# Performance work log

Measured on AMD Instinct MI355X. Metric: run time of the kernel, lower is better.

## Reference

```python
import jax, jax.numpy as jnp
import numpy as np

H = 1024
B = 8
S = 2048

def setup_inputs() -> dict:
    key = jax.random.key(0)
    ks = jax.random.split(key, 16)
    w = lambda k, shp: (jax.random.normal(k, shp, dtype=jnp.float32) * 0.02)
    return {
        "hidden_states": jax.random.normal(ks[0], (B, S, H), dtype=jnp.float32),
        "context_vector": jax.random.normal(ks[1], (B, H), dtype=jnp.float32),
        # nn.Linear weights stored torch-style as [out, in]
        "Wq": w(ks[2], (H, H)), "bq": w(ks[3], (H,)),
        "Wk": w(ks[4], (H, H)), "bk": w(ks[5], (H,)),
        "Wv": w(ks[6], (H, H)), "bv": w(ks[7], (H,)),
        "Wcq": w(ks[8], (H, H)),  # only .weight.t() used in original (no bias)
        "Wck": w(ks[9], (H, H)),
        "g_qh": jax.random.normal(ks[10], (H, 1), dtype=jnp.float32),
        "g_kh": jax.random.normal(ks[11], (H, 1), dtype=jnp.float32),
        "g_qc": jax.random.normal(ks[12], (H, 1), dtype=jnp.float32),
        "g_kc": jax.random.normal(ks[13], (H, 1), dtype=jnp.float32),
    }

def reference(hidden_states, context_vector, Wq, bq, Wk, bk, Wv, bv, Wcq, Wck, g_qh, g_kh, g_qc, g_kc):
    # Linear projections (torch Linear: x @ W.T + b)
    query = jnp.einsum('bsh,oh->bso', hidden_states, Wq) + bq   # [B,S,H]
    key_  = jnp.einsum('bsh,oh->bso', hidden_states, Wk) + bk
    value = jnp.einsum('bsh,oh->bso', hidden_states, Wv) + bv

    # gate = sigmoid(Q @ g_h + (ctx @ g_c)[:,None,:])  -> [B,S,1]
    q_gate = jax.nn.sigmoid(query @ g_qh + (context_vector @ g_qc)[:, None, :])
    k_gate = jax.nn.sigmoid(key_  @ g_kh + (context_vector @ g_kc)[:, None, :])

    # context projections: ctx @ weight.t() (no bias in original usage) -> [B,1,H]
    ctx_q = (context_vector @ Wcq.T)[:, None, :]
    ctx_k = (context_vector @ Wck.T)[:, None, :]

    query_hat = (1.0 - q_gate) * query + q_gate * ctx_q
    key_hat   = (1.0 - k_gate) * key_  + k_gate * ctx_k

    scale = 1.0 / jnp.sqrt(jnp.asarray(H, dtype=jnp.float32))
    scores = jnp.einsum('bqh,bkh->bqk', query_hat, key_hat) * scale  # [B,S,S]
    probs = jax.nn.softmax(scores, axis=-1)
    output = jnp.einsum('bqk,bkh->bqh', probs, value)  # [B,S,H]
    return (output, scores)
```

## Files before the change

kernel.cpp:

```cpp
#include <hip/hip_runtime.h>
#include <cstdint>
#include <cstddef>

#define H 1024
#define NB 8
#define S 2048
#define MROWS (NB*S)

using short8 = __attribute__((ext_vector_type(8))) short;
using f32x4  = __attribute__((ext_vector_type(4))) float;

__device__ __forceinline__ unsigned short f2bf(float f){
  union { float f; unsigned int u; } c; c.f = f;
  unsigned int u = c.u;
  return (unsigned short)((u + 0x7fffu + ((u >> 16) & 1u)) >> 16);
}


__global__ void k_cvt3(const float* __restrict__ a, const float* __restrict__ b, const float* __restrict__ c,
                       unsigned short* __restrict__ oa, unsigned short* __restrict__ ob, unsigned short* __restrict__ oc){
  const float* src = blockIdx.y == 0 ? a : (blockIdx.y == 1 ? b : c);
  unsigned short* dst = blockIdx.y == 0 ? oa : (blockIdx.y == 1 ? ob : oc);
  int i = (blockIdx.x * 256 + threadIdx.x) * 4;
  float4 v = *reinterpret_cast<const float4*>(src + i);
  ushort4 o;
  o.x = f2bf(v.x); o.y = f2bf(v.y); o.z = f2bf(v.z); o.w = f2bf(v.w);
  *reinterpret_cast<ushort4*>(dst + i) = o;
}

__global__ void k_colproj(const float* __restrict__ Wq_, const float* __restrict__ gq_,
                          const float* __restrict__ Wk_, const float* __restrict__ gk_,
                          float* __restrict__ up){
  const float* W = blockIdx.z ? Wk_ : Wq_;
  const float* g = blockIdx.z ? gk_ : gq_;
  const int in = blockIdx.x * 256 + threadIdx.x;
  const int o0 = blockIdx.y * 128;
  float s = 0.f;
  for (int o = 0; o < 128; ++o) s = fmaf(W[(size_t)(o0 + o) * H + in], g[o0 + o], s);
  up[(blockIdx.z * 8 + blockIdx.y) * 1024 + in] = s;
}

__global__ void k_ucombine(const float* __restrict__ up, float* __restrict__ uq, float* __restrict__ uk){
  int i = blockIdx.x * 256 + threadIdx.x;
  int m = i >> 10, j = i & 1023;
  float s = 0.f;
  #pragma unroll
  for (int c = 0; c < 8; ++c) s += up[(m * 8 + c) * 1024 + j];
  (m ? uk : uq)[j] = s;
}

__global__ __launch_bounds__(256) void k_ctxproj(const float* __restrict__ Wcq, const float* __restrict__ Wck,
    const float* __restrict__ ctx, float* __restrict__ outq, float* __restrict__ outk){
  __shared__ float cs[NB * H];
  const float* W = blockIdx.y ? Wck : Wcq;
  float* out = blockIdx.y ? outk : outq;
  const int t = threadIdx.x;
  for (int i = t; i < NB * H; i += 256) cs[i] = ctx[i];
  __syncthreads();
  const int wid = t >> 6, lane = t & 63;
  const int row = blockIdx.x * 4 + wid;
  float a[NB];
  #pragma unroll
  for (int b = 0; b < NB; ++b) a[b] = 0.f;
  for (int i0 = 0; i0 < H; i0 += 64){
    const float w = W[(size_t)row * H + i0 + lane];
    #pragma unroll
    for (int b = 0; b < NB; ++b) a[b] = fmaf(w, cs[b * H + i0 + lane], a[b]);
  }
  #pragma unroll
  for (int b = 0; b < NB; ++b){
    float v = a[b];
    #pragma unroll
    for (int off = 32; off > 0; off >>= 1) v += __shfl_xor(v, off);
    if (lane == 0) out[b * H + row] = v;
  }
}

__device__ float block_dot(const float* a, const float* b, float* red, int t){
  float s = 0.f;
  for (int i = t; i < H; i += 256) s = fmaf(a[i], b[i], s);
  red[t] = s;
  __syncthreads();
  for (int off = 128; off > 0; off >>= 1){
    if (t < off) red[t] += red[t + off];
    __syncthreads();
  }
  float r = red[0];
  __syncthreads();
  return r;
}

__global__ void k_scalars(const float* __restrict__ bq, const float* __restrict__ gqh,
                          const float* __restrict__ bk, const float* __restrict__ gkh,
                          const float* __restrict__ ctx, const float* __restrict__ gqc,
                          const float* __restrict__ gkc, float* __restrict__ scal){
  __shared__ float red[256];
  const int t = threadIdx.x;
  float v;
  v = block_dot(bq, gqh, red, t); if (t == 0) scal[0] = v;
  v = block_dot(bk, gkh, red, t); if (t == 0) scal[1] = v;
  for (int b = 0; b < NB; ++b){
    v = block_dot(ctx + b * H, gqc, red, t); if (t == 0) scal[2 + b] = v;
    v = block_dot(ctx + b * H, gkc, red, t); if (t == 0) scal[10 + b] = v;
  }
}

__global__ __launch_bounds__(256) void k_prepass(const float* __restrict__ hs,
    const float* __restrict__ u_q, const float* __restrict__ u_k, const float* __restrict__ scal,
    unsigned short* __restrict__ hsb, float* __restrict__ gq, float* __restrict__ gk){
  const int t = threadIdx.x, wid = t >> 6, lane = t & 63;
  const int row = blockIdx.x * 4 + wid;
  const float* hrow = hs + (size_t)row * H;
  unsigned short* orow = hsb + (size_t)row * H;
  float sq = 0.f, sk = 0.f;
  #pragma unroll
  for (int c = 0; c < 4; ++c){
    const int idx = (lane + c * 64) * 4;
    float4 v  = *reinterpret_cast<const float4*>(hrow + idx);
    float4 uq = *reinterpret_cast<const float4*>(u_q + idx);
    float4 uk = *reinterpret_cast<const float4*>(u_k + idx);
    ushort4 o; o.x = f2bf(v.x); o.y = f2bf(v.y); o.z = f2bf(v.z); o.w = f2bf(v.w);
    *reinterpret_cast<ushort4*>(orow + idx) = o;
    sq += v.x*uq.x + v.y*uq.y + v.z*uq.z + v.w*uq.w;
    sk += v.x*uk.x + v.y*uk.y + v.z*uk.z + v.w*uk.w;
  }
  #pragma unroll
  for (int off = 32; off > 0; off >>= 1){
    sq += __shfl_xor(sq, off);
    sk += __shfl_xor(sk, off);
  }
  if (lane == 0){
    const int b = row >> 11;
    gq[row] = 1.f / (1.f + __expf(-(sq + scal[0] + scal[2 + b])));
    gk[row] = 1.f / (1.f + __expf(-(sk + scal[1] + scal[10 + b])));
  }
}


#define STG(bufi, opi, halfi, koff, P0, P1) \
  { __builtin_amdgcn_global_load_lds((const __attribute__((address_space(1))) void*)(P0 + (koff)), \
      (__attribute__((address_space(3))) void*)((char*)(&lds[bufi][opi][halfi][0]) + (wid*2+0)*1024), 16, 0, 0); \
    __builtin_amdgcn_global_load_lds((const __attribute__((address_space(1))) void*)(P1 + (koff)), \
      (__attribute__((address_space(3))) void*)((char*)(&lds[bufi][opi][halfi][0]) + (wid*2+1)*1024), 16, 0, 0); }
#define STG_A(bufi, halfi, koff) STG(bufi, 0, halfi, koff, sA0, sA1)
#define STG_B(bufi, halfi, koff) STG(bufi, 1, halfi, koff, sB0, sB1)

#define DS_A(bufi, ks, mh) \
  { _Pragma("unroll") for (int m_ = 0; m_ < 4; ++m_){ \
      const int ar_ = wr*128 + ((mh)*4 + m_)*16 + (lane & 15); \
      const int sl_ = (lane >> 4) ^ ((ar_ >> 1) & 3); \
      af[m_] = *reinterpret_cast<const short8*>(&lds[bufi][0][ks][ar_*32 + sl_*8]); } }
#define DS_B(bufi, ks) \
  { _Pragma("unroll") for (int n_ = 0; n_ < 4; ++n_){ \
      const int br_ = wc*64 + n_*16 + (lane & 15); \
      const int sl_ = (lane >> 4) ^ ((br_ >> 1) & 3); \
      bf[n_] = *reinterpret_cast<const short8*>(&lds[bufi][1][ks][br_*32 + sl_*8]); } }
#define MFMA16(mh) \
  { __builtin_amdgcn_s_setprio(1); \
    _Pragma("unroll") for (int m_ = 0; m_ < 4; ++m_) \
      _Pragma("unroll") for (int n_ = 0; n_ < 4; ++n_) \
        acc[(mh)*4 + m_][n_] = __builtin_amdgcn_mfma_f32_16x16x32_bf16(af[m_], bf[n_], acc[(mh)*4 + m_][n_], 0, 0, 0); \
    __builtin_amdgcn_s_setprio(0); }
#define VM4() asm volatile("s_waitcnt vmcnt(4)" ::: "memory");
#define VM0() asm volatile("s_waitcnt vmcnt(0)" ::: "memory");
#define BAR() { asm volatile("" ::: "memory"); __builtin_amdgcn_s_barrier(); asm volatile("" ::: "memory"); }

template<int MODE>
__global__ __launch_bounds__(512, 2)
void k_gemm(const unsigned short* __restrict__ A, const unsigned short* __restrict__ B,
            int K, int ldA, int ldB, long long Abatch, long long Bbatch,
            const float* __restrict__ gate, const float* __restrict__ bias,
            const float* __restrict__ ctxv,
            unsigned short* __restrict__ outb, float* __restrict__ outf,
            long long outBatch, float scale)
{
  __shared__ __align__(16) short lds[2][2][2][8192];

  const int t = threadIdx.x;
  const int wid = t >> 6, lane = t & 63;
  const int wr = wid >> 2, wc = wid & 3;
  const int bz = blockIdx.z;
  const unsigned short* Ab = A + (size_t)bz * (size_t)Abatch;
  const unsigned short* Bb = B + (size_t)bz * (size_t)Bbatch;
  const int row0 = blockIdx.x * 256;
  const int col0 = blockIdx.y * 256;

  const int c0 = (wid*2 + 0)*64 + lane;
  const int c1 = (wid*2 + 1)*64 + lane;
  const int r0s = c0 >> 2, r1s = c1 >> 2;
  const int kc0 = (c0 & 3) ^ ((r0s >> 1) & 3);
  const int kc1 = (c1 & 3) ^ ((r1s >> 1) & 3);
  const unsigned short* sA0 = Ab + (size_t)(row0 + r0s) * (size_t)ldA + kc0*8;
  const unsigned short* sA1 = Ab + (size_t)(row0 + r1s) * (size_t)ldA + kc1*8;
  const unsigned short* sB0 = Bb + (size_t)(col0 + r0s) * (size_t)ldB + kc0*8;
  const unsigned short* sB1 = Bb + (size_t)(col0 + r1s) * (size_t)ldB + kc1*8;

  f32x4 acc[8][4] = {};
  short8 af[4], bf[4];

  STG_A(0, 0, 0); STG_B(0, 0, 0); STG_A(0, 1, 32); STG_B(0, 1, 32);
  VM0(); BAR();

  const int niter = K >> 7;
  for (int it = 0; it < niter; ++it){
    const int t1k = (it*2 + 1) << 6;
    const int t2k = (it*2 + 2) << 6;
    const bool more = (it + 1 < niter);
    DS_A(0, 0, 0); DS_B(0, 0); STG_A(1, 0, t1k); MFMA16(0); BAR();
    DS_A(0, 0, 1); STG_B(1, 0, t1k); MFMA16(1); VM4(); BAR();
    DS_A(0, 1, 0); DS_B(0, 1); STG_A(1, 1, t1k + 32); MFMA16(0); BAR();
    DS_A(0, 1, 1); STG_B(1, 1, t1k + 32); MFMA16(1);
    if (more) { VM4(); } else { VM0(); }
    BAR();
    DS_A(1, 0, 0); DS_B(1, 0); if (more) STG_A(0, 0, t2k); MFMA16(0); BAR();
    DS_A(1, 0, 1); if (more) { STG_B(0, 0, t2k); } MFMA16(1); if (more) VM4(); BAR();
    DS_A(1, 1, 0); DS_B(1, 1); if (more) STG_A(0, 1, t2k + 32); MFMA16(0); BAR();
    DS_A(1, 1, 1); if (more) { STG_B(0, 1, t2k + 32); } MFMA16(1); if (more) VM4(); BAR();
  }

  if constexpr (MODE == 0 || MODE == 1){
    const int b = row0 >> 11;
    #pragma unroll
    for (int mi = 0; mi < 8; ++mi)
      #pragma unroll
      for (int n = 0; n < 4; ++n)
        #pragma unroll
        for (int r = 0; r < 4; ++r){
          const int grow = row0 + wr*128 + mi*16 + (lane >> 4)*4 + r;
          const int gcol = col0 + wc*64 + n*16 + (lane & 15);
          const float g = gate[grow];
          const float q = acc[mi][n][r] + bias[gcol];
          outb[(size_t)grow * H + gcol] = f2bf((1.f - g) * q + g * ctxv[b * H + gcol]);
        }
  } else if constexpr (MODE == 2){
    short* tp = (short*)lds;
    const int bb = row0 >> 11;
    const int s0 = row0 & (S - 1);
    #pragma unroll
    for (int ci = 0; ci < 2; ++ci)
      #pragma unroll
      for (int cj = 0; cj < 2; ++cj){
        __syncthreads();
        if (wr == ci && (wc >> 1) == cj){
          const int lc0 = (wc & 1) * 64;
          #pragma unroll
          for (int mi = 0; mi < 8; ++mi)
            #pragma unroll
            for (int n = 0; n < 4; ++n)
              #pragma unroll
              for (int r = 0; r < 4; ++r){
                const int lr = mi*16 + (lane >> 4)*4 + r;
                const int lc = lc0 + n*16 + (lane & 15);
                tp[lr*129 + lc] = (short)f2bf(acc[mi][n][r] + bias[col0 + cj*128 + lc]);
              }
        }
        __syncthreads();
        const int hl = t >> 2;
        const int sb = (t & 3) * 32;
        unsigned short* vout = outb + (size_t)bb * H * S + (size_t)(col0 + cj*128 + hl) * S
                                    + (size_t)(s0 + ci*128 + sb);
        #pragma unroll
        for (int i2 = 0; i2 < 32; i2 += 4){
          ushort4 o;
          o.x = (unsigned short)tp[(sb + i2 + 0)*129 + hl];
          o.y = (unsigned short)tp[(sb + i2 + 1)*129 + hl];
          o.z = (unsigned short)tp[(sb + i2 + 2)*129 + hl];
          o.w = (unsigned short)tp[(sb + i2 + 3)*129 + hl];
          *reinterpret_cast<ushort4*>(vout + i2) = o;
        }
      }
  } else if constexpr (MODE == 3){
    #pragma unroll
    for (int mi = 0; mi < 8; ++mi)
      #pragma unroll
      for (int n = 0; n < 4; ++n)
        #pragma unroll
        for (int r = 0; r < 4; ++r){
          const int grow = row0 + wr*128 + mi*16 + (lane >> 4)*4 + r;
          const int gcol = col0 + wc*64 + n*16 + (lane & 15);
          outf[(size_t)bz * (size_t)outBatch + (size_t)grow * S + gcol] = acc[mi][n][r] * scale;
        }
  } else {
    #pragma unroll
    for (int mi = 0; mi < 8; ++mi)
      #pragma unroll
      for (int n = 0; n < 4; ++n)
        #pragma unroll
        for (int r = 0; r < 4; ++r){
          const int grow = row0 + wr*128 + mi*16 + (lane >> 4)*4 + r;
          const int gcol = col0 + wc*64 + n*16 + (lane & 15);
          outf[(size_t)bz * (size_t)outBatch + (size_t)grow * H + gcol] = acc[mi][n][r];
        }
  }
}

__global__ __launch_bounds__(256) void k_softmax(const float* __restrict__ scores,
                                                 unsigned short* __restrict__ probs){
  const int row = blockIdx.x;
  const float* srow = scores + (size_t)row * S;
  unsigned short* prow = probs + (size_t)row * S;
  const int t = threadIdx.x, wid = t >> 6, lane = t & 63;
  __shared__ float red[8];
  float4 v0 = *reinterpret_cast<const float4*>(srow + t * 4);
  float4 v1 = *reinterpret_cast<const float4*>(srow + 1024 + t * 4);
  float m = fmaxf(fmaxf(fmaxf(v0.x, v0.y), fmaxf(v0.z, v0.w)),
                  fmaxf(fmaxf(v1.x, v1.y), fmaxf(v1.z, v1.w)));
  #pragma unroll
  for (int off = 32; off > 0; off >>= 1) m = fmaxf(m, __shfl_xor(m, off));
  if (lane == 0) red[wid] = m;
  __syncthreads();
  m = fmaxf(fmaxf(red[0], red[1]), fmaxf(red[2], red[3]));
  float4 e0, e1;
  e0.x = __expf(v0.x - m); e0.y = __expf(v0.y - m); e0.z = __expf(v0.z - m); e0.w = __expf(v0.w - m);
  e1.x = __expf(v1.x - m); e1.y = __expf(v1.y - m); e1.z = __expf(v1.z - m); e1.w = __expf(v1.w - m);
  float s = (e0.x + e0.y + e0.z + e0.w) + (e1.x + e1.y + e1.z + e1.w);
  #pragma unroll
  for (int off = 32; off > 0; off >>= 1) s += __shfl_xor(s, off);
  if (lane == 0) red[4 + wid] = s;
  __syncthreads();
  s = (red[4] + red[5]) + (red[6] + red[7]);
  const float inv = 1.f / s;
  ushort4 o;
  o.x = f2bf(e0.x * inv); o.y = f2bf(e0.y * inv); o.z = f2bf(e0.z * inv); o.w = f2bf(e0.w * inv);
  *reinterpret_cast<ushort4*>(prow + t * 4) = o;
  o.x = f2bf(e1.x * inv); o.y = f2bf(e1.y * inv); o.z = f2bf(e1.z * inv); o.w = f2bf(e1.w * inv);
  *reinterpret_cast<ushort4*>(prow + 1024 + t * 4) = o;
}

extern "C" void kernel_launch(void* const* d_in, const int* in_sizes, int n_in,
                              void* d_out, int out_size, void* d_ws, size_t ws_size,
                              hipStream_t stream) {
  const float* hs  = (const float*)d_in[0];
  const float* ctx = (const float*)d_in[1];
  const float* Wq  = (const float*)d_in[2];
  const float* bq  = (const float*)d_in[3];
  const float* Wk  = (const float*)d_in[4];
  const float* bk  = (const float*)d_in[5];
  const float* Wv  = (const float*)d_in[6];
  const float* bv  = (const float*)d_in[7];
  const float* Wcq = (const float*)d_in[8];
  const float* Wck = (const float*)d_in[9];
  const float* gqh = (const float*)d_in[10];
  const float* gkh = (const float*)d_in[11];
  const float* gqc = (const float*)d_in[12];
  const float* gkc = (const float*)d_in[13];

  char* ws = (char*)d_ws;
  const size_t T = (size_t)MROWS * H * 2;
  unsigned short* hsb  = (unsigned short*)(ws);
  unsigned short* qhat = (unsigned short*)(ws + T);
  unsigned short* khat = (unsigned short*)(ws + 2 * T);
  unsigned short* vt   = (unsigned short*)(ws + 3 * T);
  unsigned short* wqb  = (unsigned short*)(ws + 4 * T);
  unsigned short* wkb  = (unsigned short*)(ws + 4 * T + 2097152);
  unsigned short* wvb  = (unsigned short*)(ws + 4 * T + 4194304);
  float* fb    = (float*)(ws + 4 * T + 6291456);
  float* u_q   = fb;
  float* u_k   = fb + 1024;
  float* ctxq  = fb + 2048;
  float* ctxk  = fb + 10240;
  float* gq    = fb + 18432;
  float* gk    = fb + 34816;
  float* scal  = fb + 51200;
  float* u_part= fb + 51232;
  unsigned short* probs = (unsigned short*)ws;

  float* out_attn   = (float*)d_out;
  float* out_scores = out_attn + (size_t)MROWS * H;

  k_cvt3<<<dim3(1024, 3), 256, 0, stream>>>(Wq, Wk, Wv, wqb, wkb, wvb);
  k_colproj<<<dim3(4, 8, 2), 256, 0, stream>>>(Wq, gqh, Wk, gkh, u_part);
  k_ucombine<<<8, 256, 0, stream>>>(u_part, u_q, u_k);
  k_ctxproj<<<dim3(256, 2), 256, 0, stream>>>(Wcq, Wck, ctx, ctxq, ctxk);
  k_scalars<<<1, 256, 0, stream>>>(bq, gqh, bk, gkh, ctx, gqc, gkc, scal);
  k_prepass<<<MROWS / 4, 256, 0, stream>>>(hs, u_q, u_k, scal, hsb, gq, gk);

  k_gemm<0><<<dim3(64, 4, 1), 512, 0, stream>>>(hsb, wqb, 1024, 1024, 1024, 0, 0,
      gq, bq, ctxq, qhat, nullptr, 0, 1.f);
  k_gemm<1><<<dim3(64, 4, 1), 512, 0, stream>>>(hsb, wkb, 1024, 1024, 1024, 0, 0,
      gk, bk, ctxk, khat, nullptr, 0, 1.f);
  k_gemm<2><<<dim3(64, 4, 1), 512, 0, stream>>>(hsb, wvb, 1024, 1024, 1024, 0, 0,
      nullptr, bv, nullptr, vt, nullptr, 0, 1.f);

  k_gemm<3><<<dim3(8, 8, 8), 512, 0, stream>>>(qhat, khat, 1024, 1024, 1024,
      (long long)S * H, (long long)S * H, nullptr, nullptr, nullptr,
      nullptr, out_scores, (long long)S * S, 0.03125f);

  k_softmax<<<MROWS, 256, 0, stream>>>(out_scores, probs);

  k_gemm<4><<<dim3(8, 4, 8), 512, 0, stream>>>(probs, vt, 2048, 2048, 2048,
      (long long)S * S, (long long)H * S, nullptr, nullptr, nullptr,
      nullptr, out_attn, (long long)S * H, 1.f);
}
```

Baseline: 357.0 us.

## Refactor gated QK scores algebraically via Wq^T Wk product to drop a projection GEMM

Rewrites scores = q_hat·k_hat^T by expanding the gated blends into a main term hs·(Wq^T Wk)·hs^T plus rank-one corrections built from per-row and per-column scalars. A small GEMM computes M = Wq^T Wk once, then one big GEMM forms T = hs·M, replacing the separate Q and K projection GEMMs. The scores GEMM uses hs directly as the second operand and applies the corrections in its epilogue. It adds several small precompute kernels and changes the bf16 rounding path, since hs is rounded before M is applied, which may shift numerical error.

```diff
diff --git a/kernel.cpp b/kernel.cpp
--- a/kernel.cpp
+++ b/kernel.cpp
@@ -17,10 +17,7 @@
 }
 
 
-__global__ void k_cvt3(const float* __restrict__ a, const float* __restrict__ b, const float* __restrict__ c,
-                       unsigned short* __restrict__ oa, unsigned short* __restrict__ ob, unsigned short* __restrict__ oc){
-  const float* src = blockIdx.y == 0 ? a : (blockIdx.y == 1 ? b : c);
-  unsigned short* dst = blockIdx.y == 0 ? oa : (blockIdx.y == 1 ? ob : oc);
+__global__ void k_cvt1(const float* __restrict__ src, unsigned short* __restrict__ dst){
   int i = (blockIdx.x * 256 + threadIdx.x) * 4;
   float4 v = *reinterpret_cast<const float4*>(src + i);
   ushort4 o;
@@ -28,25 +25,55 @@
   *reinterpret_cast<ushort4*>(dst + i) = o;
 }
 
-__global__ void k_colproj(const float* __restrict__ Wq_, const float* __restrict__ gq_,
-                          const float* __restrict__ Wk_, const float* __restrict__ gk_,
-                          float* __restrict__ up){
-  const float* W = blockIdx.z ? Wk_ : Wq_;
-  const float* g = blockIdx.z ? gk_ : gq_;
+__global__ __launch_bounds__(256) void k_transpose(const float* __restrict__ Wq_, const float* __restrict__ Wk_,
+    unsigned short* __restrict__ Wqt_, unsigned short* __restrict__ Wkt_){
+  const float* src = blockIdx.z ? Wk_ : Wq_;
+  unsigned short* dst = blockIdx.z ? Wkt_ : Wqt_;
+  __shared__ unsigned short tl[64][65];
+  const int t = threadIdx.x;
+  const int bx = blockIdx.x, by = blockIdx.y;
+  const int co = (t & 15) * 4;
+  #pragma unroll
+  for (int pass = 0; pass < 4; ++pass){
+    const int ro = (t >> 4) + pass * 16;
+    float4 v = *reinterpret_cast<const float4*>(src + (size_t)(by*64 + ro) * H + bx*64 + co);
+    tl[co + 0][ro] = f2bf(v.x);
+    tl[co + 1][ro] = f2bf(v.y);
+    tl[co + 2][ro] = f2bf(v.z);
+    tl[co + 3][ro] = f2bf(v.w);
+  }
+  __syncthreads();
+  #pragma unroll
+  for (int pass = 0; pass < 4; ++pass){
+    const int hh = (t >> 4) + pass * 16;
+    const int oo = (t & 15) * 4;
+    ushort4 w;
+    w.x = tl[hh][oo + 0]; w.y = tl[hh][oo + 1]; w.z = tl[hh][oo + 2]; w.w = tl[hh][oo + 3];
+    *reinterpret_cast<ushort4*>(dst + (size_t)(bx*64 + hh) * H + by*64 + oo) = w;
+  }
+}
+
+__global__ void k_colproj(const float* __restrict__ Wq_, const float* __restrict__ Wk_,
+                          const float* __restrict__ gqh, const float* __restrict__ gkh,
+                          const float* __restrict__ bq, const float* __restrict__ bk,
+                          float* __restrict__ up4){
+  const int z = blockIdx.z;
+  const float* W = (z == 0 || z == 2) ? Wq_ : Wk_;
+  const float* g = (z == 0) ? gqh : (z == 1) ? gkh : (z == 2) ? bk : bq;
   const int in = blockIdx.x * 256 + threadIdx.x;
   const int o0 = blockIdx.y * 128;
   float s = 0.f;
   for (int o = 0; o < 128; ++o) s = fmaf(W[(size_t)(o0 + o) * H + in], g[o0 + o], s);
-  up[(blockIdx.z * 8 + blockIdx.y) * 1024 + in] = s;
-}
-
-__global__ void k_ucombine(const float* __restrict__ up, float* __restrict__ uq, float* __restrict__ uk){
+  up4[(z * 8 + blockIdx.y) * 1024 + in] = s;
+}
+
+__global__ void k_ucombine4(const float* __restrict__ up4, float* __restrict__ u4){
   int i = blockIdx.x * 256 + threadIdx.x;
-  int m = i >> 10, j = i & 1023;
+  int z = i >> 10, h = i & 1023;
   float s = 0.f;
   #pragma unroll
-  for (int c = 0; c < 8; ++c) s += up[(m * 8 + c) * 1024 + j];
-  (m ? uk : uq)[j] = s;
+  for (int c = 0; c < 8; ++c) s += up4[(z * 8 + c) * 1024 + h];
+  u4[i] = s;
 }
 
 __global__ __launch_bounds__(256) void k_ctxproj(const float* __restrict__ Wcq, const float* __restrict__ Wck,
@@ -76,63 +103,114 @@
   }
 }
 
-__device__ float block_dot(const float* a, const float* b, float* red, int t){
+__global__ __launch_bounds__(256) void k_colproj8(const float* __restrict__ Wq_, const float* __restrict__ Wk_,
+    const float* __restrict__ ctxq, const float* __restrict__ ctxk, float* __restrict__ up8){
+  __shared__ float cs[NB * 128];
+  const int z = blockIdx.z;
+  const float* W = z ? Wk_ : Wq_;
+  const float* g = z ? ctxq : ctxk;
+  const int t = threadIdx.x;
+  const int o0 = blockIdx.y * 128;
+  for (int i = t; i < NB * 128; i += 256){
+    int b = i >> 7, oo = i & 127;
+    cs[i] = g[b * H + o0 + oo];
+  }
+  __syncthreads();
+  const int h = blockIdx.x * 256 + t;
+  float s[NB];
+  #pragma unroll
+  for (int b = 0; b < NB; ++b) s[b] = 0.f;
+  for (int oo = 0; oo < 128; ++oo){
+    const float w = W[(size_t)(o0 + oo) * H + h];
+    #pragma unroll
+    for (int b = 0; b < NB; ++b) s[b] = fmaf(w, cs[b * 128 + oo], s[b]);
+  }
+  #pragma unroll
+  for (int b = 0; b < NB; ++b)
+    up8[z * 65536 + blockIdx.y * 8192 + b * 1024 + h] = s[b];
+}
+
+__global__ void k_ucombine8(const float* __restrict__ up8, float* __restrict__ uXY){
+  int i = blockIdx.x * 256 + threadIdx.x;
+  int z = i >> 13, rem = i & 8191;
   float s = 0.f;
-  for (int i = t; i < H; i += 256) s = fmaf(a[i], b[i], s);
-  red[t] = s;
-  __syncthreads();
-  for (int off = 128; off > 0; off >>= 1){
-    if (t < off) red[t] += red[t + off];
-    __syncthreads();
-  }
-  float r = red[0];
-  __syncthreads();
-  return r;
-}
-
-__global__ void k_scalars(const float* __restrict__ bq, const float* __restrict__ gqh,
-                          const float* __restrict__ bk, const float* __restrict__ gkh,
-                          const float* __restrict__ ctx, const float* __restrict__ gqc,
-                          const float* __restrict__ gkc, float* __restrict__ scal){
-  __shared__ float red[256];
-  const int t = threadIdx.x;
-  float v;
-  v = block_dot(bq, gqh, red, t); if (t == 0) scal[0] = v;
-  v = block_dot(bk, gkh, red, t); if (t == 0) scal[1] = v;
-  for (int b = 0; b < NB; ++b){
-    v = block_dot(ctx + b * H, gqc, red, t); if (t == 0) scal[2 + b] = v;
-    v = block_dot(ctx + b * H, gkc, red, t); if (t == 0) scal[10 + b] = v;
+  #pragma unroll
+  for (int y = 0; y < 8; ++y) s += up8[z * 65536 + y * 8192 + rem];
+  uXY[i] = s;
+}
+
+__global__ __launch_bounds__(512) void k_scalars(const float* __restrict__ bq, const float* __restrict__ gqh,
+    const float* __restrict__ bk, const float* __restrict__ gkh,
+    const float* __restrict__ ctx, const float* __restrict__ gqc, const float* __restrict__ gkc,
+    const float* __restrict__ ctxq, const float* __restrict__ ctxk, float* __restrict__ scal){
+  const int wid = threadIdx.x >> 6, lane = threadIdx.x & 63;
+  for (int d = wid; d < 43; d += 8){
+    const float *pa, *pb;
+    if (d == 0){ pa = bq; pb = gqh; }
+    else if (d == 1){ pa = bk; pb = gkh; }
+    else if (d < 10){ pa = ctx + (d - 2) * H; pb = gqc; }
+    else if (d < 18){ pa = ctx + (d - 10) * H; pb = gkc; }
+    else if (d == 18){ pa = bq; pb = bk; }
+    else if (d < 27){ pa = bq; pb = ctxk + (d - 19) * H; }
+    else if (d < 35){ pa = ctxq + (d - 27) * H; pb = bk; }
+    else { pa = ctxq + (d - 35) * H; pb = ctxk + (d - 35) * H; }
+    float s = 0.f;
+    for (int i = lane; i < H; i += 64) s = fmaf(pa[i], pb[i], s);
+    #pragma unroll
+    for (int off = 32; off > 0; off >>= 1) s += __shfl_xor(s, off);
+    if (lane == 0) scal[d] = s;
   }
 }
 
 __global__ __launch_bounds__(256) void k_prepass(const float* __restrict__ hs,
-    const float* __restrict__ u_q, const float* __restrict__ u_k, const float* __restrict__ scal,
-    unsigned short* __restrict__ hsb, float* __restrict__ gq, float* __restrict__ gk){
+    const float* __restrict__ u4, const float* __restrict__ uXY, const float* __restrict__ scal,
+    unsigned short* __restrict__ hsb, float* __restrict__ Prow, float* __restrict__ Qcol){
   const int t = threadIdx.x, wid = t >> 6, lane = t & 63;
   const int row = blockIdx.x * 4 + wid;
+  const int b = row >> 11;
   const float* hrow = hs + (size_t)row * H;
+  const float* u_q = u4;
+  const float* u_k = u4 + 1024;
+  const float* aq  = u4 + 2048;
+  const float* ak  = u4 + 3072;
+  const float* uXb = uXY + b * 1024;
+  const float* uYb = uXY + 8192 + b * 1024;
   unsigned short* orow = hsb + (size_t)row * H;
-  float sq = 0.f, sk = 0.f;
+  float d1 = 0.f, d2 = 0.f, d3 = 0.f, d4 = 0.f, d5 = 0.f, d6 = 0.f;
   #pragma unroll
   for (int c = 0; c < 4; ++c){
     const int idx = (lane + c * 64) * 4;
     float4 v  = *reinterpret_cast<const float4*>(hrow + idx);
-    float4 uq = *reinterpret_cast<const float4*>(u_q + idx);
-    float4 uk = *reinterpret_cast<const float4*>(u_k + idx);
+    float4 a1 = *reinterpret_cast<const float4*>(u_q + idx);
+    float4 a2 = *reinterpret_cast<const float4*>(u_k + idx);
+    float4 a3 = *reinterpret_cast<const float4*>(aq + idx);
+    float4 a4 = *reinterpret_cast<const float4*>(ak + idx);
+    float4 a5 = *reinterpret_cast<const float4*>(uXb + idx);
+    float4 a6 = *reinterpret_cast<const float4*>(uYb + idx);
     ushort4 o; o.x = f2bf(v.x); o.y = f2bf(v.y); o.z = f2bf(v.z); o.w = f2bf(v.w);
     *reinterpret_cast<ushort4*>(orow + idx) = o;
-    sq += v.x*uq.x + v.y*uq.y + v.z*uq.z + v.w*uq.w;
-    sk += v.x*uk.x + v.y*uk.y + v.z*uk.z + v.w*uk.w;
+    d1 += v.x*a1.x + v.y*a1.y + v.z*a1.z + v.w*a1.w;
+    d2 += v.x*a2.x + v.y*a2.y + v.z*a2.z + v.w*a2.w;
+    d3 += v.x*a3.x + v.y*a3.y + v.z*a3.z + v.w*a3.w;
+    d4 += v.x*a4.x + v.y*a4.y + v.z*a4.z + v.w*a4.w;
+    d5 += v.x*a5.x + v.y*a5.y + v.z*a5.z + v.w*a5.w;
+    d6 += v.x*a6.x + v.y*a6.y + v.z*a6.z + v.w*a6.w;
   }
   #pragma unroll
   for (int off = 32; off > 0; off >>= 1){
-    sq += __shfl_xor(sq, off);
-    sk += __shfl_xor(sk, off);
+    d1 += __shfl_xor(d1, off); d2 += __shfl_xor(d2, off); d3 += __shfl_xor(d3, off);
+    d4 += __shfl_xor(d4, off); d5 += __shfl_xor(d5, off); d6 += __shfl_xor(d6, off);
   }
   if (lane == 0){
-    const int b = row >> 11;
-    gq[row] = 1.f / (1.f + __expf(-(sq + scal[0] + scal[2 + b])));
-    gk[row] = 1.f / (1.f + __expf(-(sk + scal[1] + scal[10 + b])));
+    float gqv = 1.f / (1.f + __expf(-(d1 + scal[0] + scal[2 + b])));
+    float gkv = 1.f / (1.f + __expf(-(d2 + scal[1] + scal[10 + b])));
+    float X = d5 + scal[19 + b];
+    float Y = d6 + scal[27 + b];
+    float eq = 1.f - gqv, ek = 1.f - gkv;
+    float4 P; P.x = eq; P.y = eq * (d3 + scal[18]); P.z = eq * X; P.w = gqv;
+    float4 Q; Q.x = ek; Q.y = ek * d4; Q.z = gkv; Q.w = ek * Y + gkv * scal[35 + b];
+    reinterpret_cast<float4*>(Prow)[row] = P;
+    reinterpret_cast<float4*>(Qcol)[row] = Q;
   }
 }
 
@@ -218,8 +296,7 @@
     DS_A(1, 1, 1); if (more) { STG_B(0, 1, t2k + 32); } MFMA16(1); if (more) VM4(); BAR();
   }
 
-  if constexpr (MODE == 0 || MODE == 1){
-    const int b = row0 >> 11;
+  if constexpr (MODE == 0){
     #pragma unroll
     for (int mi = 0; mi < 8; ++mi)
       #pragma unroll
@@ -228,9 +305,7 @@
         for (int r = 0; r < 4; ++r){
           const int grow = row0 + wr*128 + mi*16 + (lane >> 4)*4 + r;
           const int gcol = col0 + wc*64 + n*16 + (lane & 15);
-          const float g = gate[grow];
-          const float q = acc[mi][n][r] + bias[gcol];
-          outb[(size_t)grow * H + gcol] = f2bf((1.f - g) * q + g * ctxv[b * H + gcol]);
+          outb[(size_t)grow * H + gcol] = f2bf(acc[mi][n][r]);
         }
   } else if constexpr (MODE == 2){
     short* tp = (short*)lds;
@@ -270,16 +345,37 @@
         }
       }
   } else if constexpr (MODE == 3){
+    float* PQ = (float*)lds;
+    __syncthreads();
+    if (t < 256){
+      float4 p = reinterpret_cast<const float4*>(gate)[(size_t)bz * S + row0 + t];
+      PQ[t] = p.x; PQ[256 + t] = p.y; PQ[512 + t] = p.z; PQ[768 + t] = p.w;
+    } else if (t < 512){
+      const int j = t - 256;
+      float4 q = reinterpret_cast<const float4*>(ctxv)[(size_t)bz * S + col0 + j];
+      PQ[1024 + j] = q.x; PQ[1280 + j] = q.y; PQ[1536 + j] = q.z; PQ[1792 + j] = q.w;
+    }
+    __syncthreads();
+    float q1[4], q2[4], q3[4], q4[4];
+    #pragma unroll
+    for (int n = 0; n < 4; ++n){
+      const int lc = wc*64 + n*16 + (lane & 15);
+      q1[n] = PQ[1024 + lc]; q2[n] = PQ[1280 + lc]; q3[n] = PQ[1536 + lc]; q4[n] = PQ[1792 + lc];
+    }
     #pragma unroll
     for (int mi = 0; mi < 8; ++mi)
       #pragma unroll
-      for (int n = 0; n < 4; ++n)
+      for (int r = 0; r < 4; ++r){
+        const int lr = wr*128 + mi*16 + (lane >> 4)*4 + r;
+        const float p1 = PQ[lr], p2 = PQ[256 + lr], p3 = PQ[512 + lr], p4 = PQ[768 + lr];
         #pragma unroll
-        for (int r = 0; r < 4; ++r){
-          const int grow = row0 + wr*128 + mi*16 + (lane >> 4)*4 + r;
+        for (int n = 0; n < 4; ++n){
           const int gcol = col0 + wc*64 + n*16 + (lane & 15);
-          outf[(size_t)bz * (size_t)outBatch + (size_t)grow * S + gcol] = acc[mi][n][r] * scale;
+          const float g = acc[mi][n][r];
+          const float val = q1[n] * fmaf(p1, g, p2) + p1 * q2[n] + p3 * q3[n] + p4 * q4[n];
+          outf[(size_t)bz * (size_t)outBatch + (size_t)(row0 + lr) * S + gcol] = scale * val;
         }
+      }
   } else {
     #pragma unroll
     for (int mi = 0; mi < 8; ++mi)
@@ -292,6 +388,18 @@
           outf[(size_t)bz * (size_t)outBatch + (size_t)grow * H + gcol] = acc[mi][n][r];
         }
   }
+}
+
+__global__ void k_mreduce(const float* __restrict__ mpart, unsigned short* __restrict__ Mt){
+  const int i4 = (blockIdx.x * 256 + threadIdx.x) * 4;
+  float4 s = *reinterpret_cast<const float4*>(mpart + i4);
+  #pragma unroll
+  for (int kz = 1; kz < 4; ++kz){
+    float4 p = *reinterpret_cast<const float4*>(mpart + (size_t)kz * 1048576 + i4);
+    s.x += p.x; s.y += p.y; s.z += p.z; s.w += p.w;
+  }
+  ushort4 o; o.x = f2bf(s.x); o.y = f2bf(s.y); o.z = f2bf(s.z); o.w = f2bf(s.w);
+  *reinterpret_cast<ushort4*>(Mt + i4) = o;
 }
 
 __global__ __launch_bounds__(256) void k_softmax(const float* __restrict__ scores,
@@ -346,44 +454,50 @@
   const float* gkc = (const float*)d_in[13];
 
   char* ws = (char*)d_ws;
-  const size_t T = (size_t)MROWS * H * 2;
   unsigned short* hsb  = (unsigned short*)(ws);
-  unsigned short* qhat = (unsigned short*)(ws + T);
-  unsigned short* khat = (unsigned short*)(ws + 2 * T);
-  unsigned short* vt   = (unsigned short*)(ws + 3 * T);
-  unsigned short* wqb  = (unsigned short*)(ws + 4 * T);
-  unsigned short* wkb  = (unsigned short*)(ws + 4 * T + 2097152);
-  unsigned short* wvb  = (unsigned short*)(ws + 4 * T + 4194304);
-  float* fb    = (float*)(ws + 4 * T + 6291456);
-  float* u_q   = fb;
-  float* u_k   = fb + 1024;
-  float* ctxq  = fb + 2048;
-  float* ctxk  = fb + 10240;
-  float* gq    = fb + 18432;
-  float* gk    = fb + 34816;
-  float* scal  = fb + 51200;
-  float* u_part= fb + 51232;
+  unsigned short* Tb   = (unsigned short*)(ws + 33554432);
+  unsigned short* vt   = (unsigned short*)(ws + 67108864);
+  unsigned short* wvb  = (unsigned short*)(ws + 100663296);
+  unsigned short* wqt  = (unsigned short*)(ws + 102760448);
+  unsigned short* wkt  = (unsigned short*)(ws + 104857600);
+  unsigned short* mt   = (unsigned short*)(ws + 106954752);
+  float* mpart = (float*)(ws + 109051904);
+  float* up4   = (float*)(ws + 125829120);
+  float* u4    = (float*)(ws + 125960192);
+  float* up8   = (float*)(ws + 125976576);
+  float* uXY   = (float*)(ws + 126500864);
+  float* ctxq  = (float*)(ws + 126566400);
+  float* ctxk  = (float*)(ws + 126599168);
+  float* scal  = (float*)(ws + 126631936);
+  float* Prow  = (float*)(ws + 126632192);
+  float* Qcol  = (float*)(ws + 126894336);
   unsigned short* probs = (unsigned short*)ws;
 
   float* out_attn   = (float*)d_out;
   float* out_scores = out_attn + (size_t)MROWS * H;
 
-  k_cvt3<<<dim3(1024, 3), 256, 0, stream>>>(Wq, Wk, Wv, wqb, wkb, wvb);
-  k_colproj<<<dim3(4, 8, 2), 256, 0, stream>>>(Wq, gqh, Wk, gkh, u_part);
-  k_ucombine<<<8, 256, 0, stream>>>(u_part, u_q, u_k);
+  k_transpose<<<dim3(16, 16, 2), 256, 0, stream>>>(Wq, Wk, wqt, wkt);
+  k_cvt1<<<1024, 256, 0, stream>>>(Wv, wvb);
   k_ctxproj<<<dim3(256, 2), 256, 0, stream>>>(Wcq, Wck, ctx, ctxq, ctxk);
-  k_scalars<<<1, 256, 0, stream>>>(bq, gqh, bk, gkh, ctx, gqc, gkc, scal);
-  k_prepass<<<MROWS / 4, 256, 0, stream>>>(hs, u_q, u_k, scal, hsb, gq, gk);
-
-  k_gemm<0><<<dim3(64, 4, 1), 512, 0, stream>>>(hsb, wqb, 1024, 1024, 1024, 0, 0,
-      gq, bq, ctxq, qhat, nullptr, 0, 1.f);
-  k_gemm<1><<<dim3(64, 4, 1), 512, 0, stream>>>(hsb, wkb, 1024, 1024, 1024, 0, 0,
-      gk, bk, ctxk, khat, nullptr, 0, 1.f);
+  k_colproj<<<dim3(4, 8, 4), 256, 0, stream>>>(Wq, Wk, gqh, gkh, bq, bk, up4);
+  k_ucombine4<<<16, 256, 0, stream>>>(up4, u4);
+  k_colproj8<<<dim3(4, 8, 2), 256, 0, stream>>>(Wq, Wk, ctxq, ctxk, up8);
+  k_ucombine8<<<64, 256, 0, stream>>>(up8, uXY);
+  k_scalars<<<1, 512, 0, stream>>>(bq, gqh, bk, gkh, ctx, gqc, gkc, ctxq, ctxk, scal);
+  k_prepass<<<MROWS / 4, 256, 0, stream>>>(hs, u4, uXY, scal, hsb, Prow, Qcol);
+
+  k_gemm<4><<<dim3(4, 4, 4), 512, 0, stream>>>(wkt, wqt, 256, 1024, 1024, 256, 256,
+      nullptr, nullptr, nullptr, nullptr, mpart, 1048576LL, 1.f);
+  k_mreduce<<<1024, 256, 0, stream>>>(mpart, mt);
+
+  k_gemm<0><<<dim3(64, 4, 1), 512, 0, stream>>>(hsb, mt, 1024, 1024, 1024, 0, 0,
+      nullptr, nullptr, nullptr, Tb, nullptr, 0, 1.f);
+
   k_gemm<2><<<dim3(64, 4, 1), 512, 0, stream>>>(hsb, wvb, 1024, 1024, 1024, 0, 0,
       nullptr, bv, nullptr, vt, nullptr, 0, 1.f);
 
-  k_gemm<3><<<dim3(8, 8, 8), 512, 0, stream>>>(qhat, khat, 1024, 1024, 1024,
-      (long long)S * H, (long long)S * H, nullptr, nullptr, nullptr,
+  k_gemm<3><<<dim3(8, 8, 8), 512, 0, stream>>>(Tb, hsb, 1024, 1024, 1024,
+      (long long)S * H, (long long)S * H, Prow, nullptr, Qcol,
       nullptr, out_scores, (long long)S * S, 0.03125f);
 
   k_softmax<<<MROWS, 256, 0, stream>>>(out_scores, probs);
```

Result: slower. 365.0 us (+2.2%).
